# Optimization experiments

Measured on AMD Instinct MI355X. Metric: run time of the kernel, lower is better.

The kernel has to match this reference:

```python
import jax, jax.numpy as jnp
import numpy as np

B, N, C, H = 4, 1024, 512, 8
HD = C // H
SCALE = HD ** -0.5
LN_EPS = 1e-5


def setup_inputs() -> dict:
    key = jax.random.key(0)
    ks = jax.random.split(key, 4)
    return {
        "x": jax.random.normal(ks[0], (B, N, C), dtype=jnp.float32),
        "Wqkv": jax.random.normal(ks[1], (C, 3 * C), dtype=jnp.float32) * (C ** -0.5),
        "bqkv": jnp.zeros((3 * C,), dtype=jnp.float32),
        "order_weights": jnp.ones((3,), dtype=jnp.float32),
        "Wproj": jax.random.normal(ks[2], (C, C), dtype=jnp.float32) * (C ** -0.5),
        "bproj": jnp.zeros((C,), dtype=jnp.float32),
        "gamma": jnp.ones((C,), dtype=jnp.float32),
        "beta": jnp.zeros((C,), dtype=jnp.float32),
    }


def reference(x, Wqkv, bqkv, order_weights, Wproj, bproj, gamma, beta):
    b, n, c = x.shape
    qkv = (x @ Wqkv + bqkv).reshape(b, n, 3, H, HD)
    qkv = jnp.transpose(qkv, (2, 0, 3, 1, 4))  # [3, B, H, N, HD]
    q, k, v = qkv[0], qkv[1], qkv[2]

    base = jnp.einsum('bhnd,bhmd->bhnm', q, k) * SCALE  # [B, H, N, N]

    ow = jax.nn.softmax(order_weights)
    # torch loop: term_0 = base, term_i = base**(i+1)
    attn = ow[0] * base
    cur = base
    for i in range(1, order_weights.shape[0]):
        cur = cur * base
        attn = attn + ow[i] * cur

    attn_final = jax.nn.softmax(attn, axis=-1)

    out = jnp.einsum('bhnm,bhmd->bhnd', attn_final, v)
    out = jnp.transpose(out, (0, 2, 1, 3)).reshape(b, n, c)
    out = out @ Wproj + bproj

    y = x + out
    mu = jnp.mean(y, axis=-1, keepdims=True)
    var = jnp.var(y, axis=-1, keepdims=True)
    y = (y - mu) / jnp.sqrt(var + LN_EPS) * gamma + beta
    return y, attn_final
```

## Files before the change

### kernel.cpp

```cpp
#include <hip/hip_runtime.h>
#include <math.h>

#define B_ 4
#define N_ 1024
#define C_ 512
#define H_ 8
#define HD_ 64
#define SCALE_ 0.125f
#define LN_EPS_ 1e-5f

__global__ __launch_bounds__(256) void qkv_gemm(const float* __restrict__ x,
                                                const float* __restrict__ Wqkv,
                                                const float* __restrict__ bqkv,
                                                float* __restrict__ qkv) {
    const int K = C_;
    const int NN = 3 * C_;
    __shared__ float As[64][17];
    __shared__ float Bs[16][64];

    const int tid = threadIdx.x;
    const int tx = tid & 15;
    const int ty = tid >> 4;
    const int row0 = blockIdx.y * 64;
    const int col0 = blockIdx.x * 64;

    float acc[4][4] = {};

    for (int kt = 0; kt < K; kt += 16) {
        {
            int lin = tid * 4;
            int m = lin >> 4;
            int k = lin & 15;
            float4 a = *(const float4*)&x[(size_t)(row0 + m) * K + kt + k];
            As[m][k + 0] = a.x; As[m][k + 1] = a.y;
            As[m][k + 2] = a.z; As[m][k + 3] = a.w;
        }
        {
            int lin = tid * 4;
            int kk = lin >> 6;
            int n = lin & 63;
            *(float4*)&Bs[kk][n] =
                *(const float4*)&Wqkv[(size_t)(kt + kk) * NN + col0 + n];
        }
        __syncthreads();
#pragma unroll
        for (int kk = 0; kk < 16; ++kk) {
            float a[4], bb[4];
#pragma unroll
            for (int i = 0; i < 4; ++i) a[i] = As[ty * 4 + i][kk];
#pragma unroll
            for (int j = 0; j < 4; ++j) bb[j] = Bs[kk][tx * 4 + j];
#pragma unroll
            for (int i = 0; i < 4; ++i)
#pragma unroll
                for (int j = 0; j < 4; ++j) acc[i][j] += a[i] * bb[j];
        }
        __syncthreads();
    }
#pragma unroll
    for (int i = 0; i < 4; ++i) {
        int r = row0 + ty * 4 + i;
        int c = col0 + tx * 4;
        float4 o;
        o.x = acc[i][0] + bqkv[c + 0];
        o.y = acc[i][1] + bqkv[c + 1];
        o.z = acc[i][2] + bqkv[c + 2];
        o.w = acc[i][3] + bqkv[c + 3];
        *(float4*)&qkv[(size_t)r * NN + c] = o;
    }
}

__global__ __launch_bounds__(256) void attn_scores(const float* __restrict__ qkv,
                                                   const float* __restrict__ ow_in,
                                                   float* __restrict__ attn) {
    __shared__ __align__(16) float Qst[64][20];
    __shared__ __align__(16) float Kst[16][264];

    const int tid = threadIdx.x;
    const int lane = tid & 63;
    const int ry = tid >> 6;
    const int n0 = blockIdx.x * 16;
    const int bh = blockIdx.y;
    const int b = bh >> 3, h = bh & 7;
    const size_t RS = 3 * C_;

    float w0 = ow_in[0], w1 = ow_in[1], w2 = ow_in[2];
    float wm = fmaxf(w0, fmaxf(w1, w2));
    float e0 = __expf(w0 - wm), e1 = __expf(w1 - wm), e2 = __expf(w2 - wm);
    float einv = 1.0f / (e0 + e1 + e2);
    float ow0 = e0 * einv, ow1 = e1 * einv, ow2 = e2 * einv;

    {
        int r = tid >> 4, f = tid & 15;
        const float* qrow = qkv + (size_t)(b * N_ + n0 + r) * RS + h * HD_;
        float4 qv = ((const float4*)qrow)[f];
        Qst[f * 4 + 0][r] = qv.x; Qst[f * 4 + 1][r] = qv.y;
        Qst[f * 4 + 2][r] = qv.z; Qst[f * 4 + 3][r] = qv.w;
    }

    float s[4][16];
    float lmax[4] = {-1e30f, -1e30f, -1e30f, -1e30f};

#pragma unroll
    for (int ct = 0; ct < 4; ++ct) {
#pragma unroll
        for (int u = 0; u < 16; ++u) s[ct][u] = 0.f;
#pragma unroll
        for (int kc = 0; kc < 4; ++kc) {
            const float* krow =
                qkv + (size_t)(b * N_ + ct * 256 + tid) * RS + C_ + h * HD_ + kc * 16;
            float4 kv0 = ((const float4*)krow)[0];
            float4 kv1 = ((const float4*)krow)[1];
            float4 kv2 = ((const float4*)krow)[2];
            float4 kv3 = ((const float4*)krow)[3];
            __syncthreads();
            Kst[ 0][tid] = kv0.x; Kst[ 1][tid] = kv0.y; Kst[ 2][tid] = kv0.z; Kst[ 3][tid] = kv0.w;
            Kst[ 4][tid] = kv1.x; Kst[ 5][tid] = kv1.y; Kst[ 6][tid] = kv1.z; Kst[ 7][tid] = kv1.w;
            Kst[ 8][tid] = kv2.x; Kst[ 9][tid] = kv2.y; Kst[10][tid] = kv2.z; Kst[11][tid] = kv2.w;
            Kst[12][tid] = kv3.x; Kst[13][tid] = kv3.y; Kst[14][tid] = kv3.z; Kst[15][tid] = kv3.w;
            __syncthreads();
#pragma unroll
            for (int kk = 0; kk < 16; ++kk) {
                float4 a4 = *(const float4*)&Qst[kc * 16 + kk][ry * 4];
                float4 b4 = *(const float4*)&Kst[kk][lane * 4];
                float a[4] = {a4.x, a4.y, a4.z, a4.w};
                float bb[4] = {b4.x, b4.y, b4.z, b4.w};
#pragma unroll
                for (int i = 0; i < 4; ++i)
#pragma unroll
                    for (int jj = 0; jj < 4; ++jj)
                        s[ct][i * 4 + jj] += a[i] * bb[jj];
            }
        }
#pragma unroll
        for (int i = 0; i < 4; ++i)
#pragma unroll
            for (int jj = 0; jj < 4; ++jj) {
                float sc = s[ct][i * 4 + jj] * SCALE_;
                float l = sc * (ow0 + sc * (ow1 + sc * ow2));
                s[ct][i * 4 + jj] = l;
                lmax[i] = fmaxf(lmax[i], l);
            }
    }

#pragma unroll
    for (int i = 0; i < 4; ++i)
#pragma unroll
        for (int m = 1; m < 64; m <<= 1)
            lmax[i] = fmaxf(lmax[i], __shfl_xor(lmax[i], m, 64));

    float lsum[4] = {0.f, 0.f, 0.f, 0.f};
#pragma unroll
    for (int ct = 0; ct < 4; ++ct)
#pragma unroll
        for (int i = 0; i < 4; ++i)
#pragma unroll
            for (int jj = 0; jj < 4; ++jj) {
                float e = __expf(s[ct][i * 4 + jj] - lmax[i]);
                s[ct][i * 4 + jj] = e;
                lsum[i] += e;
            }
#pragma unroll
    for (int i = 0; i < 4; ++i)
#pragma unroll
        for (int m = 1; m < 64; m <<= 1)
            lsum[i] += __shfl_xor(lsum[i], m, 64);

    float inv[4];
#pragma unroll
    for (int i = 0; i < 4; ++i) inv[i] = 1.0f / lsum[i];

#pragma unroll
    for (int ct = 0; ct < 4; ++ct)
#pragma unroll
        for (int i = 0; i < 4; ++i) {
            float4 p;
            p.x = s[ct][i * 4 + 0] * inv[i];
            p.y = s[ct][i * 4 + 1] * inv[i];
            p.z = s[ct][i * 4 + 2] * inv[i];
            p.w = s[ct][i * 4 + 3] * inv[i];
            *(float4*)&attn[((size_t)bh * N_ + n0 + ry * 4 + i) * N_ + ct * 256 + lane * 4] = p;
        }
}

__global__ __launch_bounds__(256) void pv_gemm(const float* __restrict__ qkv,
                                               const float* __restrict__ attn,
                                               float* __restrict__ ctx) {
    __shared__ __align__(16) float Pst[64][68];
    __shared__ __align__(16) float Vs[64][68];

    const int tid = threadIdx.x;
    const int tx = tid & 15;
    const int ty = tid >> 4;
    const int n0 = blockIdx.x * 64;
    const int bh = blockIdx.y;
    const int b = bh >> 3, h = bh & 7;
    const size_t RS = 3 * C_;

    const int rr = tid >> 2;
    const int q = tid & 3;

    float acc[4][4] = {};

    for (int mt = 0; mt < 16; ++mt) {
        const int m0 = mt * 64;
        const float* prow = attn + ((size_t)bh * N_ + n0 + rr) * N_ + m0 + q * 16;
        const float* vrow = qkv + (size_t)(b * N_ + m0 + rr) * RS + 2 * C_ + h * HD_ + q * 16;
        float4 pv[4], vv[4];
#pragma unroll
        for (int m = 0; m < 4; ++m) pv[m] = ((const float4*)prow)[m];
#pragma unroll
        for (int m = 0; m < 4; ++m) vv[m] = ((const float4*)vrow)[m];
        __syncthreads();
#pragma unroll
        for (int m = 0; m < 4; ++m) {
            int c = q * 16 + m * 4;
            Pst[c + 0][rr] = pv[m].x; Pst[c + 1][rr] = pv[m].y;
            Pst[c + 2][rr] = pv[m].z; Pst[c + 3][rr] = pv[m].w;
            *(float4*)&Vs[rr][c] = vv[m];
        }
        __syncthreads();
#pragma unroll 16
        for (int mm = 0; mm < 64; ++mm) {
            float4 a4 = *(const float4*)&Pst[mm][ty * 4];
            float4 b4 = *(const float4*)&Vs[mm][tx * 4];
            float a[4] = {a4.x, a4.y, a4.z, a4.w};
            float bb[4] = {b4.x, b4.y, b4.z, b4.w};
#pragma unroll
            for (int i = 0; i < 4; ++i)
#pragma unroll
                for (int j = 0; j < 4; ++j) acc[i][j] += a[i] * bb[j];
        }
    }
#pragma unroll
    for (int i = 0; i < 4; ++i) {
        float4 o;
        o.x = acc[i][0]; o.y = acc[i][1]; o.z = acc[i][2]; o.w = acc[i][3];
        *(float4*)&ctx[(size_t)(b * N_ + n0 + ty * 4 + i) * C_ + h * HD_ + tx * 4] = o;
    }
}

__global__ __launch_bounds__(256) void proj_gemm(const float* __restrict__ ctx,
                                                 const float* __restrict__ x,
                                                 const float* __restrict__ Wproj,
                                                 const float* __restrict__ bproj,
                                                 float* __restrict__ y) {
    const int K = C_;
    const int NN = C_;
    __shared__ float As[64][17];
    __shared__ float Bs[16][64];

    const int tid = threadIdx.x;
    const int tx = tid & 15;
    const int ty = tid >> 4;
    const int row0 = blockIdx.y * 64;
    const int col0 = blockIdx.x * 64;

    float acc[4][4] = {};

    for (int kt = 0; kt < K; kt += 16) {
        {
            int lin = tid * 4;
            int m = lin >> 4;
            int k = lin & 15;
            float4 a = *(const float4*)&ctx[(size_t)(row0 + m) * K + kt + k];
            As[m][k + 0] = a.x; As[m][k + 1] = a.y;
            As[m][k + 2] = a.z; As[m][k + 3] = a.w;
        }
        {
            int lin = tid * 4;
            int kk = lin >> 6;
            int n = lin & 63;
            *(float4*)&Bs[kk][n] =
                *(const float4*)&Wproj[(size_t)(kt + kk) * NN + col0 + n];
        }
        __syncthreads();
#pragma unroll
        for (int kk = 0; kk < 16; ++kk) {
            float a[4], bb[4];
#pragma unroll
            for (int i = 0; i < 4; ++i) a[i] = As[ty * 4 + i][kk];
#pragma unroll
            for (int j = 0; j < 4; ++j) bb[j] = Bs[kk][tx * 4 + j];
#pragma unroll
            for (int i = 0; i < 4; ++i)
#pragma unroll
                for (int j = 0; j < 4; ++j) acc[i][j] += a[i] * bb[j];
        }
        __syncthreads();
    }
#pragma unroll
    for (int i = 0; i < 4; ++i) {
        int r = row0 + ty * 4 + i;
        int c = col0 + tx * 4;
        float4 xr = *(const float4*)&x[(size_t)r * C_ + c];
        float4 o;
        o.x = acc[i][0] + bproj[c + 0] + xr.x;
        o.y = acc[i][1] + bproj[c + 1] + xr.y;
        o.z = acc[i][2] + bproj[c + 2] + xr.z;
        o.w = acc[i][3] + bproj[c + 3] + xr.w;
        *(float4*)&y[(size_t)r * C_ + c] = o;
    }
}

__global__ __launch_bounds__(256) void ln_kernel(float* __restrict__ y,
                                                 const float* __restrict__ gamma,
                                                 const float* __restrict__ beta) {
    __shared__ float wsum[4], wsq[4];
    const int row = blockIdx.x;
    const int tid = threadIdx.x;
    const int lane = tid & 63;
    const int w = tid >> 6;

    float2 v = ((const float2*)(y + (size_t)row * C_))[tid];
    float s = v.x + v.y;
    float sq = v.x * v.x + v.y * v.y;
#pragma unroll
    for (int m = 1; m < 64; m <<= 1) {
        s += __shfl_xor(s, m, 64);
        sq += __shfl_xor(sq, m, 64);
    }
    if (lane == 0) { wsum[w] = s; wsq[w] = sq; }
    __syncthreads();
    float ts = wsum[0] + wsum[1] + wsum[2] + wsum[3];
    float tq = wsq[0] + wsq[1] + wsq[2] + wsq[3];
    float mu = ts * (1.0f / C_);
    float var = tq * (1.0f / C_) - mu * mu;
    float rstd = rsqrtf(var + LN_EPS_);

    float2 g = ((const float2*)gamma)[tid];
    float2 be = ((const float2*)beta)[tid];
    float2 o;
    o.x = (v.x - mu) * rstd * g.x + be.x;
    o.y = (v.y - mu) * rstd * g.y + be.y;
    ((float2*)(y + (size_t)row * C_))[tid] = o;
}

extern "C" void kernel_launch(void* const* d_in, const int* in_sizes, int n_in,
                              void* d_out, int out_size, void* d_ws, size_t ws_size,
                              hipStream_t stream) {
    const float* x     = (const float*)d_in[0];
    const float* Wqkv  = (const float*)d_in[1];
    const float* bqkv  = (const float*)d_in[2];
    const float* ow    = (const float*)d_in[3];
    const float* Wproj = (const float*)d_in[4];
    const float* bproj = (const float*)d_in[5];
    const float* gamma = (const float*)d_in[6];
    const float* beta  = (const float*)d_in[7];

    float* out  = (float*)d_out;
    float* y    = out;
    float* attn = out + (size_t)B_ * N_ * C_;
    float* qkv  = (float*)d_ws;
    float* ctx  = qkv + (size_t)B_ * N_ * 3 * C_;

    dim3 g1(3 * C_ / 64, B_ * N_ / 64);
    qkv_gemm<<<g1, 256, 0, stream>>>(x, Wqkv, bqkv, qkv);

    dim3 g2(N_ / 16, B_ * H_);
    attn_scores<<<g2, 256, 0, stream>>>(qkv, ow, attn);

    dim3 g3(N_ / 64, B_ * H_);
    pv_gemm<<<g3, 256, 0, stream>>>(qkv, attn, ctx);

    dim3 g4(C_ / 64, B_ * N_ / 64);
    proj_gemm<<<g4, 256, 0, stream>>>(ctx, x, Wproj, bproj, y);

    ln_kernel<<<B_ * N_, 256, 0, stream>>>(y, gamma, beta);
}
```

Baseline: 467.9 us.

## Compute attention scores with split-fp16 MFMA instead of scalar FP32 FMAs

Rewrites the QK^T score kernel to use 16x16x32 fp16 MFMA instructions. Q and K are split into hi/lo fp16 pairs and three MFMAs per chunk approximate fp32 precision. K is loaded directly from global memory per wave instead of being staged through LDS. The row softmax is now reduced across waves via shared memory. The attn stores become scalar 16-strided writes rather than float4, which may reduce store efficiency on the large attention output.

```diff
diff --git a/kernel.cpp b/kernel.cpp
--- a/kernel.cpp
+++ b/kernel.cpp
@@ -8,6 +8,20 @@
 #define HD_ 64
 #define SCALE_ 0.125f
 #define LN_EPS_ 1e-5f
+
+typedef _Float16 f16x8 __attribute__((ext_vector_type(8)));
+typedef float f32x4 __attribute__((ext_vector_type(4)));
+
+__device__ __forceinline__ void cvt_split(const float4& A, const float4& Bv,
+                                          f16x8& hi, f16x8& lo) {
+    float v[8] = {A.x, A.y, A.z, A.w, Bv.x, Bv.y, Bv.z, Bv.w};
+#pragma unroll
+    for (int i = 0; i < 8; ++i) {
+        _Float16 h = (_Float16)v[i];
+        hi[i] = h;
+        lo[i] = (_Float16)(v[i] - (float)h);
+    }
+}
 
 __global__ __launch_bounds__(256) void qkv_gemm(const float* __restrict__ x,
                                                 const float* __restrict__ Wqkv,
@@ -73,12 +87,14 @@
 __global__ __launch_bounds__(256) void attn_scores(const float* __restrict__ qkv,
                                                    const float* __restrict__ ow_in,
                                                    float* __restrict__ attn) {
-    __shared__ __align__(16) float Qst[64][20];
-    __shared__ __align__(16) float Kst[16][264];
+    __shared__ float smax[4][16];
+    __shared__ float ssum[4][16];
 
     const int tid = threadIdx.x;
     const int lane = tid & 63;
-    const int ry = tid >> 6;
+    const int w = tid >> 6;
+    const int r16 = lane & 15;
+    const int g = lane >> 4;
     const int n0 = blockIdx.x * 16;
     const int bh = blockIdx.y;
     const int b = bh >> 3, h = bh & 7;
@@ -90,97 +106,105 @@
     float einv = 1.0f / (e0 + e1 + e2);
     float ow0 = e0 * einv, ow1 = e1 * einv, ow2 = e2 * einv;
 
+    const float* qrow = qkv + (size_t)(b * N_ + n0 + r16) * RS + h * HD_;
+    f16x8 aHi0, aLo0, aHi1, aLo1;
     {
-        int r = tid >> 4, f = tid & 15;
-        const float* qrow = qkv + (size_t)(b * N_ + n0 + r) * RS + h * HD_;
-        float4 qv = ((const float4*)qrow)[f];
-        Qst[f * 4 + 0][r] = qv.x; Qst[f * 4 + 1][r] = qv.y;
-        Qst[f * 4 + 2][r] = qv.z; Qst[f * 4 + 3][r] = qv.w;
-    }
-
-    float s[4][16];
-    float lmax[4] = {-1e30f, -1e30f, -1e30f, -1e30f};
-
-#pragma unroll
-    for (int ct = 0; ct < 4; ++ct) {
-#pragma unroll
-        for (int u = 0; u < 16; ++u) s[ct][u] = 0.f;
-#pragma unroll
-        for (int kc = 0; kc < 4; ++kc) {
-            const float* krow =
-                qkv + (size_t)(b * N_ + ct * 256 + tid) * RS + C_ + h * HD_ + kc * 16;
-            float4 kv0 = ((const float4*)krow)[0];
-            float4 kv1 = ((const float4*)krow)[1];
-            float4 kv2 = ((const float4*)krow)[2];
-            float4 kv3 = ((const float4*)krow)[3];
-            __syncthreads();
-            Kst[ 0][tid] = kv0.x; Kst[ 1][tid] = kv0.y; Kst[ 2][tid] = kv0.z; Kst[ 3][tid] = kv0.w;
-            Kst[ 4][tid] = kv1.x; Kst[ 5][tid] = kv1.y; Kst[ 6][tid] = kv1.z; Kst[ 7][tid] = kv1.w;
-            Kst[ 8][tid] = kv2.x; Kst[ 9][tid] = kv2.y; Kst[10][tid] = kv2.z; Kst[11][tid] = kv2.w;
-            Kst[12][tid] = kv3.x; Kst[13][tid] = kv3.y; Kst[14][tid] = kv3.z; Kst[15][tid] = kv3.w;
-            __syncthreads();
-#pragma unroll
-            for (int kk = 0; kk < 16; ++kk) {
-                float4 a4 = *(const float4*)&Qst[kc * 16 + kk][ry * 4];
-                float4 b4 = *(const float4*)&Kst[kk][lane * 4];
-                float a[4] = {a4.x, a4.y, a4.z, a4.w};
-                float bb[4] = {b4.x, b4.y, b4.z, b4.w};
-#pragma unroll
-                for (int i = 0; i < 4; ++i)
-#pragma unroll
-                    for (int jj = 0; jj < 4; ++jj)
-                        s[ct][i * 4 + jj] += a[i] * bb[jj];
-            }
-        }
-#pragma unroll
-        for (int i = 0; i < 4; ++i)
-#pragma unroll
-            for (int jj = 0; jj < 4; ++jj) {
-                float sc = s[ct][i * 4 + jj] * SCALE_;
-                float l = sc * (ow0 + sc * (ow1 + sc * ow2));
-                s[ct][i * 4 + jj] = l;
-                lmax[i] = fmaxf(lmax[i], l);
-            }
-    }
-
-#pragma unroll
-    for (int i = 0; i < 4; ++i)
-#pragma unroll
-        for (int m = 1; m < 64; m <<= 1)
-            lmax[i] = fmaxf(lmax[i], __shfl_xor(lmax[i], m, 64));
-
-    float lsum[4] = {0.f, 0.f, 0.f, 0.f};
-#pragma unroll
-    for (int ct = 0; ct < 4; ++ct)
-#pragma unroll
-        for (int i = 0; i < 4; ++i)
-#pragma unroll
-            for (int jj = 0; jj < 4; ++jj) {
-                float e = __expf(s[ct][i * 4 + jj] - lmax[i]);
-                s[ct][i * 4 + jj] = e;
-                lsum[i] += e;
-            }
-#pragma unroll
-    for (int i = 0; i < 4; ++i)
-#pragma unroll
-        for (int m = 1; m < 64; m <<= 1)
-            lsum[i] += __shfl_xor(lsum[i], m, 64);
-
+        float4 qa = ((const float4*)qrow)[2 * g + 0];
+        float4 qb = ((const float4*)qrow)[2 * g + 1];
+        float4 qc = ((const float4*)qrow)[8 + 2 * g];
+        float4 qd = ((const float4*)qrow)[9 + 2 * g];
+        cvt_split(qa, qb, aHi0, aLo0);
+        cvt_split(qc, qd, aHi1, aLo1);
+    }
+
+    float p[16][4];
+
+    const float* kbase = qkv + (size_t)(b * N_) * RS + C_ + h * HD_;
+#pragma unroll
+    for (int t = 0; t < 16; ++t) {
+        const int ct = w * 16 + t;
+        const float* krow = kbase + (size_t)(ct * 16 + r16) * RS;
+        float4 ka = ((const float4*)krow)[2 * g + 0];
+        float4 kb = ((const float4*)krow)[2 * g + 1];
+        float4 kc = ((const float4*)krow)[8 + 2 * g];
+        float4 kd = ((const float4*)krow)[9 + 2 * g];
+        f16x8 bHi0, bLo0, bHi1, bLo1;
+        cvt_split(ka, kb, bHi0, bLo0);
+        cvt_split(kc, kd, bHi1, bLo1);
+
+        f32x4 acc = {0.f, 0.f, 0.f, 0.f};
+        acc = __builtin_amdgcn_mfma_f32_16x16x32_f16(aHi0, bHi0, acc, 0, 0, 0);
+        acc = __builtin_amdgcn_mfma_f32_16x16x32_f16(aHi0, bLo0, acc, 0, 0, 0);
+        acc = __builtin_amdgcn_mfma_f32_16x16x32_f16(aLo0, bHi0, acc, 0, 0, 0);
+        acc = __builtin_amdgcn_mfma_f32_16x16x32_f16(aHi1, bHi1, acc, 0, 0, 0);
+        acc = __builtin_amdgcn_mfma_f32_16x16x32_f16(aHi1, bLo1, acc, 0, 0, 0);
+        acc = __builtin_amdgcn_mfma_f32_16x16x32_f16(aLo1, bHi1, acc, 0, 0, 0);
+
+#pragma unroll
+        for (int j = 0; j < 4; ++j) {
+            float s = acc[j] * SCALE_;
+            p[t][j] = s * (ow0 + s * (ow1 + s * ow2));
+        }
+    }
+
+    float rmax[4] = {-1e30f, -1e30f, -1e30f, -1e30f};
+#pragma unroll
+    for (int t = 0; t < 16; ++t)
+#pragma unroll
+        for (int j = 0; j < 4; ++j) rmax[j] = fmaxf(rmax[j], p[t][j]);
+#pragma unroll
+    for (int j = 0; j < 4; ++j)
+#pragma unroll
+        for (int m = 1; m < 16; m <<= 1)
+            rmax[j] = fmaxf(rmax[j], __shfl_xor(rmax[j], m, 64));
+    if (r16 == 0) {
+#pragma unroll
+        for (int j = 0; j < 4; ++j) smax[w][g * 4 + j] = rmax[j];
+    }
+    __syncthreads();
+    float gm[4];
+#pragma unroll
+    for (int j = 0; j < 4; ++j) {
+        int rr = g * 4 + j;
+        gm[j] = fmaxf(fmaxf(smax[0][rr], smax[1][rr]),
+                      fmaxf(smax[2][rr], smax[3][rr]));
+    }
+
+    float rsum[4] = {0.f, 0.f, 0.f, 0.f};
+#pragma unroll
+    for (int t = 0; t < 16; ++t)
+#pragma unroll
+        for (int j = 0; j < 4; ++j) {
+            float e = __expf(p[t][j] - gm[j]);
+            p[t][j] = e;
+            rsum[j] += e;
+        }
+#pragma unroll
+    for (int j = 0; j < 4; ++j)
+#pragma unroll
+        for (int m = 1; m < 16; m <<= 1)
+            rsum[j] += __shfl_xor(rsum[j], m, 64);
+    if (r16 == 0) {
+#pragma unroll
+        for (int j = 0; j < 4; ++j) ssum[w][g * 4 + j] = rsum[j];
+    }
+    __syncthreads();
     float inv[4];
 #pragma unroll
-    for (int i = 0; i < 4; ++i) inv[i] = 1.0f / lsum[i];
-
-#pragma unroll
-    for (int ct = 0; ct < 4; ++ct)
-#pragma unroll
-        for (int i = 0; i < 4; ++i) {
-            float4 p;
-            p.x = s[ct][i * 4 + 0] * inv[i];
-            p.y = s[ct][i * 4 + 1] * inv[i];
-            p.z = s[ct][i * 4 + 2] * inv[i];
-            p.w = s[ct][i * 4 + 3] * inv[i];
-            *(float4*)&attn[((size_t)bh * N_ + n0 + ry * 4 + i) * N_ + ct * 256 + lane * 4] = p;
-        }
+    for (int j = 0; j < 4; ++j) {
+        int rr = g * 4 + j;
+        inv[j] = 1.0f / (ssum[0][rr] + ssum[1][rr] + ssum[2][rr] + ssum[3][rr]);
+    }
+
+    float* abase = attn + ((size_t)bh * N_ + n0 + 4 * g) * N_ + w * 256 + r16;
+#pragma unroll
+    for (int j = 0; j < 4; ++j) {
+        float* arow = abase + (size_t)j * N_;
+        float sc = inv[j];
+#pragma unroll
+        for (int t = 0; t < 16; ++t)
+            arow[t * 16] = p[t][j] * sc;
+    }
 }
 
 __global__ __launch_bounds__(256) void pv_gemm(const float* __restrict__ qkv,
```

After: 441.1 us. 5.7% less time.
